# Optimization experiments

Hardware: AMD Instinct MI355X
Metric: run time of the kernel (lower is better)

Reference implementation:

```python
import jax, jax.numpy as jnp
import numpy as np

KEEP_RATIO = 0.5
TEMPERATURE = 1.0
MIN_GATE = 0.0
EPS = 1e-06


def setup_inputs() -> dict:
    key = jax.random.key(0)
    k1, k2 = jax.random.split(key)
    B, C = 8192, 4096
    token = jax.random.normal(k1, (B, C), dtype=jnp.float32)
    proxy = jax.random.normal(k2, (B, C), dtype=jnp.float32)
    return {"token": token, "proxy": proxy}


def reference(token, proxy):
    tok = token  # [B, C]
    px = jax.lax.stop_gradient(proxy)  # detach_proxy=True
    score = jnp.abs(tok * px)  # [B, C]
    B, C = score.shape
    k = max(1, int(round(C * KEEP_RATIO)))
    # hard mask: top-k indices per row -> scatter 1.0
    _, topk_idx = jax.lax.top_k(score, k)  # [B, k]
    rows = jnp.arange(B)[:, None]
    hard_mask = jnp.zeros_like(score).at[rows, topk_idx].set(1.0)
    # per-row standardization (torch.std is unbiased -> ddof=1)
    mu = jnp.mean(score, axis=-1, keepdims=True)
    sigma = jnp.maximum(jnp.std(score, axis=-1, ddof=1, keepdims=True), EPS)
    z = (score - mu) / sigma / max(TEMPERATURE, EPS)
    soft_gate = jax.nn.sigmoid(z)
    if MIN_GATE > 0:
        soft_gate = soft_gate * (1.0 - MIN_GATE) + MIN_GATE
    gate = soft_gate * (1.0 - hard_mask) + hard_mask
    return tok * gate
```

## Files before the change

kernel.cpp:

```cpp
#include <hip/hip_runtime.h>
#include <math.h>

#define CLS   4096
#define KSEL  2048u
#define TPB   256

typedef float f32x4 __attribute__((ext_vector_type(4)));


__device__ __forceinline__ int h0slot(unsigned b) {
    unsigned j = b & 7u, t = b >> 3;
    return (int)((j << 8) | ((t + 4u*j) & 255u));
}

template<int SHIFT, int NBITS, int BPL>
__device__ __forceinline__ void radix_small(const float sc[16], unsigned* hist,
        int lane, unsigned& prefix, unsigned& kr, unsigned& cnt_eq)
{
    const unsigned msk = (1u << NBITS) - 1u;
    #pragma unroll
    for (int i = 0; i < 16; ++i) {
        unsigned u = __float_as_uint(sc[i]);
        if ((u >> (SHIFT + NBITS)) == (prefix >> (SHIFT + NBITS)))
            atomicAdd(&hist[(u >> SHIFT) & msk], 1u);
    }
    __syncthreads();
    unsigned c[BPL];
    if constexpr (BPL == 4) {
        uint4 x = *(const uint4*)&hist[lane * 4];
        c[0] = x.x; c[1] = x.y; c[2] = x.z; c[3] = x.w;
    } else {
        c[0] = hist[lane];
    }
    unsigned sfx[BPL + 1]; sfx[BPL] = 0;
    #pragma unroll
    for (int j = BPL - 1; j >= 0; --j) sfx[j] = sfx[j + 1] + c[j];
    const unsigned tot = sfx[0];
    unsigned s = tot;
    #pragma unroll
    for (int off = 1; off < 64; off <<= 1) {
        unsigned t = __shfl_down(s, off);
        if (lane + off < 64) s += t;
    }
    const unsigned Sx = s - tot;
    const bool has = (Sx < kr) && (kr <= Sx + tot);
    unsigned bin = 0, below = 0, ceq = 0;
    if (has) {
        #pragma unroll
        for (int j = 0; j < BPL; ++j)
            if (Sx + sfx[j] >= kr && Sx + sfx[j + 1] < kr) {
                bin = (unsigned)(lane * BPL + j);
                below = Sx + sfx[j + 1];
                ceq = c[j];
            }
    }
    unsigned long long m = __ballot(has);
    int src = (int)__builtin_ctzll(m);
    bin = __shfl(bin, src); below = __shfl(below, src); ceq = __shfl(ceq, src);
    prefix |= bin << SHIFT;
    kr -= below;
    cnt_eq = ceq;
}

__global__ __launch_bounds__(TPB) void proxy_gate_kernel(
    const float* __restrict__ token,
    const float* __restrict__ proxy,
    float* __restrict__ out)
{
    __shared__ __align__(16) unsigned char lds[18816];
    unsigned* h0    = (unsigned*)(lds);
    unsigned* cand  = (unsigned*)(lds + 16416);
    unsigned* h1    = (unsigned*)(lds + 16416);
    unsigned* h2    = (unsigned*)(lds + 17456);
    unsigned* h3    = (unsigned*)(lds + 18496);
    unsigned* s_cnt = (unsigned*)(lds + 18752);
    unsigned* s_wt  = (unsigned*)(lds + 18756);
    unsigned* s_bc  = (unsigned*)(lds + 18772);
    float*    s_fr  = (float*)   (lds + 18784);
    unsigned char* s_flag = lds;
    unsigned*      s_suf  = (unsigned*)(lds + 8192);

    const int tid  = threadIdx.x;
    const int lane = tid & 63;
    const int wv   = tid >> 6;
    const size_t base = (size_t)blockIdx.x * CLS;
    const float4* t4 = (const float4*)(token + base);
    const float4* p4 = (const float4*)(proxy + base);
    f32x4* o4 = (f32x4*)(out + base);

    float4 tv[4], pv[4];
    #pragma unroll
    for (int i = 0; i < 4; ++i) { tv[i] = t4[i*TPB + tid]; pv[i] = p4[i*TPB + tid]; }
    {
        uint4 z = make_uint4(0u, 0u, 0u, 0u);
        uint4* zp = (uint4*)lds;
        #pragma unroll
        for (int m = 0; m < 5; ++m) { int idx = m*TPB + tid; if (idx < 1154) zp[idx] = z; }
        if (tid == 0) *s_cnt = 0u;
    }

    float tok[16], sc[16];
    float sum = 0.f, sumsq = 0.f;
    #pragma unroll
    for (int i = 0; i < 4; ++i) {
        float a;
        a = fabsf(tv[i].x*pv[i].x); tok[i*4+0]=tv[i].x; sc[i*4+0]=a; sum+=a; sumsq+=a*a;
        a = fabsf(tv[i].y*pv[i].y); tok[i*4+1]=tv[i].y; sc[i*4+1]=a; sum+=a; sumsq+=a*a;
        a = fabsf(tv[i].z*pv[i].z); tok[i*4+2]=tv[i].z; sc[i*4+2]=a; sum+=a; sumsq+=a*a;
        a = fabsf(tv[i].w*pv[i].w); tok[i*4+3]=tv[i].w; sc[i*4+3]=a; sum+=a; sumsq+=a*a;
    }
    __syncthreads();

    {
        unsigned* h0c = h0 + (((tid >> 2) & 1) ? 2052 : 0);
        #pragma unroll
        for (int i = 0; i < 16; ++i)
            atomicAdd(&h0c[h0slot(__float_as_uint(sc[i]) >> 20)], 1u);
    }
    #pragma unroll
    for (int off = 32; off > 0; off >>= 1) {
        sum   += __shfl_xor(sum, off);
        sumsq += __shfl_xor(sumsq, off);
    }
    if (lane == 0) { s_fr[wv] = sum; s_fr[4+wv] = sumsq; }
    __syncthreads();

    const float tot_s = s_fr[0]+s_fr[1]+s_fr[2]+s_fr[3];
    const float tot_q = s_fr[4]+s_fr[5]+s_fr[6]+s_fr[7];
    const float mu = tot_s * (1.0f/CLS);
    float var = (tot_q - tot_s*mu) * (1.0f/(CLS-1));
    var = fmaxf(var, 0.0f);
    const float inv_sigma = 1.0f / fmaxf(sqrtf(var), 1e-6f);

    unsigned kr = KSEL;
    {
        unsigned c[8];
        #pragma unroll
        for (int j = 0; j < 8; ++j) {
            int sl = (j << 8) | ((tid + 4*j) & 255);
            c[j] = h0[sl] + h0[2052 + sl];
        }
        unsigned sfx[9]; sfx[8] = 0;
        #pragma unroll
        for (int j = 7; j >= 0; --j) sfx[j] = sfx[j+1] + c[j];
        const unsigned tot = sfx[0];
        unsigned s = tot;
        #pragma unroll
        for (int off = 1; off < 64; off <<= 1) {
            unsigned t = __shfl_down(s, off);
            if (lane + off < 64) s += t;
        }
        if (lane == 0) s_wt[wv] = s;
        __syncthreads();
        unsigned addhi = 0;
        #pragma unroll
        for (int w2 = 0; w2 < 4; ++w2) if (w2 > wv) addhi += s_wt[w2];
        const unsigned Sx = (s - tot) + addhi;
        if (Sx < kr && kr <= Sx + tot) {
            #pragma unroll
            for (int j = 0; j < 8; ++j)
                if (Sx + sfx[j] >= kr && Sx + sfx[j+1] < kr) {
                    s_bc[0] = (unsigned)(tid*8 + j);
                    s_bc[1] = Sx + sfx[j+1];
                    s_bc[2] = c[j];
                }
        }
        __syncthreads();
        kr -= s_bc[1];
    }
    const unsigned bin = s_bc[0];
    unsigned cnt_eq = s_bc[2];

    {
        unsigned cmask = 0, lc = 0;
        #pragma unroll
        for (int ii = 0; ii < 16; ++ii) {
            bool cnd = ((__float_as_uint(sc[ii]) >> 20) == bin);
            cmask |= ((unsigned)cnd) << ii;
            lc += (unsigned)cnd;
        }
        unsigned inc = lc;
        #pragma unroll
        for (int off = 1; off < 64; off <<= 1) {
            unsigned t = __shfl_up(inc, off);
            if (lane >= off) inc += t;
        }
        const unsigned wtot = __shfl(inc, 63);
        unsigned wbase = 0;
        if (lane == 0) wbase = atomicAdd(s_cnt, wtot);
        wbase = __shfl(wbase, 0);
        unsigned p = wbase + (inc - lc);
        #pragma unroll
        for (int ii = 0; ii < 16; ++ii) {
            if ((cmask >> ii) & 1u) {
                unsigned u = __float_as_uint(sc[ii]);
                unsigned idx = (unsigned)((ii >> 2)*1024 + tid*4 + (ii & 3));
                if (p < 512u) cand[p] = ((u & 0xFFFFFu) << 12) | (4095u - idx);
                ++p;
            }
        }
    }
    __syncthreads();
    const unsigned cnt = *s_cnt;
    const bool cand_mode = (cnt <= 512u);

    float thr = 0.f; bool tie_rare = false;
    if (cand_mode) {
        #pragma unroll
        for (int rpt = 0; rpt < 2; ++rpt) {
            const unsigned slot = (unsigned)tid + (unsigned)rpt*256u;
            if (slot < cnt) {
                const unsigned my = cand[slot];
                unsigned rank = 0;
                const uint4* c4 = (const uint4*)cand;
                const unsigned nq = (cnt + 3u) >> 2;
                for (unsigned q = 0; q < nq; ++q) {
                    uint4 v = c4[q];
                    rank += (unsigned)(v.x > my) + (unsigned)(v.y > my)
                          + (unsigned)(v.z > my) + (unsigned)(v.w > my);
                }
                if (rank == kr - 1u) s_bc[0] = my;
            }
        }
    } else {
        unsigned prefix = bin << 20;
        {
            unsigned* hz = (unsigned*)(lds + 16416);
            #pragma unroll
            for (int m = 0; m < 3; ++m) { int ix = m*TPB + tid; if (ix < 584) hz[ix] = 0u; }
        }
        __syncthreads();
        radix_small<12, 8, 4>(sc, h1, lane, prefix, kr, cnt_eq);
        radix_small< 4, 8, 4>(sc, h2, lane, prefix, kr, cnt_eq);
        radix_small< 0, 4, 1>(sc, h3, lane, prefix, kr, cnt_eq);
        thr = __uint_as_float(prefix);
        tie_rare = (cnt_eq != kr);
        if (tie_rare) {
            #pragma unroll
            for (int i = 0; i < 4; ++i)
                #pragma unroll
                for (int c2 = 0; c2 < 4; ++c2)
                    s_flag[i*1024 + tid*4 + c2] = (sc[i*4+c2] == thr) ? 1 : 0;
            __syncthreads();
            unsigned lc = 0;
            unsigned char mf[16];
            #pragma unroll
            for (int m = 0; m < 16; ++m) { mf[m] = s_flag[tid*16 + m]; lc += mf[m]; }
            s_suf[tid] = lc;
            __syncthreads();
            #pragma unroll
            for (int off = 1; off < 256; off <<= 1) {
                unsigned w = s_suf[tid] + ((tid >= off) ? s_suf[tid - off] : 0u);
                __syncthreads();
                s_suf[tid] = w;
                __syncthreads();
            }
            unsigned r = s_suf[tid] - lc;
            #pragma unroll
            for (int m = 0; m < 16; ++m) {
                if (mf[m]) { s_flag[tid*16 + m] = (r < kr) ? 2 : 0; ++r; }
            }
        }
    }
    __syncthreads();
    const unsigned Kth = s_bc[0];

    #pragma unroll
    for (int i = 0; i < 4; ++i) {
        float res[4];
        #pragma unroll
        for (int c2 = 0; c2 < 4; ++c2) {
            const float s = sc[i*4+c2];
            const float z = (s - mu) * inv_sigma;
            const float soft = 1.0f / (1.0f + __expf(-z));
            bool hard;
            const unsigned u = __float_as_uint(s);
            if (cand_mode) {
                const unsigned e = u >> 20;
                const unsigned idx = (unsigned)(i*1024 + tid*4 + c2);
                const unsigned packed = ((u & 0xFFFFFu) << 12) | (4095u - idx);
                hard = (e > bin) || ((e == bin) && (packed >= Kth));
            } else if (tie_rare) {
                hard = (s > thr) || ((s == thr) && (s_flag[i*1024 + tid*4 + c2] == 2));
            } else {
                hard = (s >= thr);
            }
            res[c2] = tok[i*4+c2] * (hard ? 1.0f : soft);
        }
        f32x4 rv = { res[0], res[1], res[2], res[3] };
        __builtin_nontemporal_store(rv, &o4[i*TPB + tid]);
    }
}

extern "C" void kernel_launch(void* const* d_in, const int* in_sizes, int n_in,
                              void* d_out, int out_size, void* d_ws, size_t ws_size,
                              hipStream_t stream) {
    const float* token = (const float*)d_in[0];
    const float* proxy = (const float*)d_in[1];
    float* outp = (float*)d_out;
    const int B = in_sizes[0] / CLS;
    hipLaunchKernelGGL(proxy_gate_kernel, dim3(B), dim3(TPB), 0, stream,
                       token, proxy, outp);
}
```

Measured before the change: 72.65 us.

## Process eight rows per block with register prefetch of next row

Each block now loops over eight rows instead of one. While the current row is being processed, it loads the next row's token and proxy into registers, so global-memory latency overlaps with the LDS-heavy top-k selection. The grid shrinks from 8192 blocks to 1024, which reduces parallelism and latency hiding across blocks. The extra prefetch registers may also lower occupancy.

Result: slower. 121.1 us (+66.7%).

```diff
diff --git a/kernel.cpp b/kernel.cpp
--- a/kernel.cpp
+++ b/kernel.cpp
@@ -4,6 +4,7 @@
 #define CLS   4096
 #define KSEL  2048u
 #define TPB   256
+#define ROWS  8
 
 typedef float f32x4 __attribute__((ext_vector_type(4)));
 
@@ -65,7 +66,8 @@
 __global__ __launch_bounds__(TPB) void proxy_gate_kernel(
     const float* __restrict__ token,
     const float* __restrict__ proxy,
-    float* __restrict__ out)
+    float* __restrict__ out,
+    int nrows)
 {
     __shared__ __align__(16) unsigned char lds[18816];
     unsigned* h0    = (unsigned*)(lds);
@@ -83,14 +85,15 @@
     const int tid  = threadIdx.x;
     const int lane = tid & 63;
     const int wv   = tid >> 6;
-    const size_t base = (size_t)blockIdx.x * CLS;
-    const float4* t4 = (const float4*)(token + base);
-    const float4* p4 = (const float4*)(proxy + base);
-    f32x4* o4 = (f32x4*)(out + base);
+    const int row0 = blockIdx.x * ROWS;
 
     float4 tv[4], pv[4];
-    #pragma unroll
-    for (int i = 0; i < 4; ++i) { tv[i] = t4[i*TPB + tid]; pv[i] = p4[i*TPB + tid]; }
+    {
+        const float4* t4 = (const float4*)(token + (size_t)row0 * CLS);
+        const float4* p4 = (const float4*)(proxy + (size_t)row0 * CLS);
+        #pragma unroll
+        for (int i = 0; i < 4; ++i) { tv[i] = t4[i*TPB + tid]; pv[i] = p4[i*TPB + tid]; }
+    }
     {
         uint4 z = make_uint4(0u, 0u, 0u, 0u);
         uint4* zp = (uint4*)lds;
@@ -99,196 +102,223 @@
         if (tid == 0) *s_cnt = 0u;
     }
 
-    float tok[16], sc[16];
-    float sum = 0.f, sumsq = 0.f;
-    #pragma unroll
-    for (int i = 0; i < 4; ++i) {
-        float a;
-        a = fabsf(tv[i].x*pv[i].x); tok[i*4+0]=tv[i].x; sc[i*4+0]=a; sum+=a; sumsq+=a*a;
-        a = fabsf(tv[i].y*pv[i].y); tok[i*4+1]=tv[i].y; sc[i*4+1]=a; sum+=a; sumsq+=a*a;
-        a = fabsf(tv[i].z*pv[i].z); tok[i*4+2]=tv[i].z; sc[i*4+2]=a; sum+=a; sumsq+=a*a;
-        a = fabsf(tv[i].w*pv[i].w); tok[i*4+3]=tv[i].w; sc[i*4+3]=a; sum+=a; sumsq+=a*a;
-    }
-    __syncthreads();
-
-    {
-        unsigned* h0c = h0 + (((tid >> 2) & 1) ? 2052 : 0);
-        #pragma unroll
-        for (int i = 0; i < 16; ++i)
-            atomicAdd(&h0c[h0slot(__float_as_uint(sc[i]) >> 20)], 1u);
-    }
-    #pragma unroll
-    for (int off = 32; off > 0; off >>= 1) {
-        sum   += __shfl_xor(sum, off);
-        sumsq += __shfl_xor(sumsq, off);
-    }
-    if (lane == 0) { s_fr[wv] = sum; s_fr[4+wv] = sumsq; }
-    __syncthreads();
-
-    const float tot_s = s_fr[0]+s_fr[1]+s_fr[2]+s_fr[3];
-    const float tot_q = s_fr[4]+s_fr[5]+s_fr[6]+s_fr[7];
-    const float mu = tot_s * (1.0f/CLS);
-    float var = (tot_q - tot_s*mu) * (1.0f/(CLS-1));
-    var = fmaxf(var, 0.0f);
-    const float inv_sigma = 1.0f / fmaxf(sqrtf(var), 1e-6f);
-
-    unsigned kr = KSEL;
-    {
-        unsigned c[8];
-        #pragma unroll
-        for (int j = 0; j < 8; ++j) {
-            int sl = (j << 8) | ((tid + 4*j) & 255);
-            c[j] = h0[sl] + h0[2052 + sl];
-        }
-        unsigned sfx[9]; sfx[8] = 0;
-        #pragma unroll
-        for (int j = 7; j >= 0; --j) sfx[j] = sfx[j+1] + c[j];
-        const unsigned tot = sfx[0];
-        unsigned s = tot;
-        #pragma unroll
-        for (int off = 1; off < 64; off <<= 1) {
-            unsigned t = __shfl_down(s, off);
-            if (lane + off < 64) s += t;
-        }
-        if (lane == 0) s_wt[wv] = s;
+    for (int r = 0; r < ROWS; ++r) {
+        const int row = row0 + r;
+        if (row >= nrows) break;
+        const bool pf = (r + 1 < ROWS) && (row + 1 < nrows);
+
+        float4 ntv[4], npv[4];
+        if (pf) {
+            const float4* t4 = (const float4*)(token + (size_t)(row+1) * CLS);
+            const float4* p4 = (const float4*)(proxy + (size_t)(row+1) * CLS);
+            #pragma unroll
+            for (int i = 0; i < 4; ++i) { ntv[i] = t4[i*TPB + tid]; npv[i] = p4[i*TPB + tid]; }
+        }
+
+        float sc[16];
+        float sum = 0.f, sumsq = 0.f;
+        #pragma unroll
+        for (int i = 0; i < 4; ++i) {
+            float a;
+            a = fabsf(tv[i].x*pv[i].x); sc[i*4+0]=a; sum+=a; sumsq+=a*a;
+            a = fabsf(tv[i].y*pv[i].y); sc[i*4+1]=a; sum+=a; sumsq+=a*a;
+            a = fabsf(tv[i].z*pv[i].z); sc[i*4+2]=a; sum+=a; sumsq+=a*a;
+            a = fabsf(tv[i].w*pv[i].w); sc[i*4+3]=a; sum+=a; sumsq+=a*a;
+        }
         __syncthreads();
-        unsigned addhi = 0;
-        #pragma unroll
-        for (int w2 = 0; w2 < 4; ++w2) if (w2 > wv) addhi += s_wt[w2];
-        const unsigned Sx = (s - tot) + addhi;
-        if (Sx < kr && kr <= Sx + tot) {
-            #pragma unroll
-            for (int j = 0; j < 8; ++j)
-                if (Sx + sfx[j] >= kr && Sx + sfx[j+1] < kr) {
-                    s_bc[0] = (unsigned)(tid*8 + j);
-                    s_bc[1] = Sx + sfx[j+1];
-                    s_bc[2] = c[j];
-                }
-        }
+
+        {
+            unsigned* h0c = h0 + (((tid >> 2) & 1) ? 2052 : 0);
+            #pragma unroll
+            for (int i = 0; i < 16; ++i)
+                atomicAdd(&h0c[h0slot(__float_as_uint(sc[i]) >> 20)], 1u);
+        }
+        #pragma unroll
+        for (int off = 32; off > 0; off >>= 1) {
+            sum   += __shfl_xor(sum, off);
+            sumsq += __shfl_xor(sumsq, off);
+        }
+        if (lane == 0) { s_fr[wv] = sum; s_fr[4+wv] = sumsq; }
         __syncthreads();
-        kr -= s_bc[1];
-    }
-    const unsigned bin = s_bc[0];
-    unsigned cnt_eq = s_bc[2];
-
-    {
-        unsigned cmask = 0, lc = 0;
-        #pragma unroll
-        for (int ii = 0; ii < 16; ++ii) {
-            bool cnd = ((__float_as_uint(sc[ii]) >> 20) == bin);
-            cmask |= ((unsigned)cnd) << ii;
-            lc += (unsigned)cnd;
-        }
-        unsigned inc = lc;
-        #pragma unroll
-        for (int off = 1; off < 64; off <<= 1) {
-            unsigned t = __shfl_up(inc, off);
-            if (lane >= off) inc += t;
-        }
-        const unsigned wtot = __shfl(inc, 63);
-        unsigned wbase = 0;
-        if (lane == 0) wbase = atomicAdd(s_cnt, wtot);
-        wbase = __shfl(wbase, 0);
-        unsigned p = wbase + (inc - lc);
-        #pragma unroll
-        for (int ii = 0; ii < 16; ++ii) {
-            if ((cmask >> ii) & 1u) {
-                unsigned u = __float_as_uint(sc[ii]);
-                unsigned idx = (unsigned)((ii >> 2)*1024 + tid*4 + (ii & 3));
-                if (p < 512u) cand[p] = ((u & 0xFFFFFu) << 12) | (4095u - idx);
-                ++p;
-            }
-        }
-    }
-    __syncthreads();
-    const unsigned cnt = *s_cnt;
-    const bool cand_mode = (cnt <= 512u);
-
-    float thr = 0.f; bool tie_rare = false;
-    if (cand_mode) {
-        #pragma unroll
-        for (int rpt = 0; rpt < 2; ++rpt) {
-            const unsigned slot = (unsigned)tid + (unsigned)rpt*256u;
-            if (slot < cnt) {
-                const unsigned my = cand[slot];
-                unsigned rank = 0;
-                const uint4* c4 = (const uint4*)cand;
-                const unsigned nq = (cnt + 3u) >> 2;
-                for (unsigned q = 0; q < nq; ++q) {
-                    uint4 v = c4[q];
-                    rank += (unsigned)(v.x > my) + (unsigned)(v.y > my)
-                          + (unsigned)(v.z > my) + (unsigned)(v.w > my);
-                }
-                if (rank == kr - 1u) s_bc[0] = my;
-            }
-        }
-    } else {
-        unsigned prefix = bin << 20;
+
+        const float tot_s = s_fr[0]+s_fr[1]+s_fr[2]+s_fr[3];
+        const float tot_q = s_fr[4]+s_fr[5]+s_fr[6]+s_fr[7];
+        const float mu = tot_s * (1.0f/CLS);
+        float var = (tot_q - tot_s*mu) * (1.0f/(CLS-1));
+        var = fmaxf(var, 0.0f);
+        const float inv_sigma = 1.0f / fmaxf(sqrtf(var), 1e-6f);
+
+        unsigned kr = KSEL;
         {
-            unsigned* hz = (unsigned*)(lds + 16416);
-            #pragma unroll
-            for (int m = 0; m < 3; ++m) { int ix = m*TPB + tid; if (ix < 584) hz[ix] = 0u; }
+            unsigned c[8];
+            #pragma unroll
+            for (int j = 0; j < 8; ++j) {
+                int sl = (j << 8) | ((tid + 4*j) & 255);
+                c[j] = h0[sl] + h0[2052 + sl];
+            }
+            unsigned sfx[9]; sfx[8] = 0;
+            #pragma unroll
+            for (int j = 7; j >= 0; --j) sfx[j] = sfx[j+1] + c[j];
+            const unsigned tot = sfx[0];
+            unsigned s = tot;
+            #pragma unroll
+            for (int off = 1; off < 64; off <<= 1) {
+                unsigned t = __shfl_down(s, off);
+                if (lane + off < 64) s += t;
+            }
+            if (lane == 0) s_wt[wv] = s;
+            __syncthreads();
+            unsigned addhi = 0;
+            #pragma unroll
+            for (int w2 = 0; w2 < 4; ++w2) if (w2 > wv) addhi += s_wt[w2];
+            const unsigned Sx = (s - tot) + addhi;
+            if (Sx < kr && kr <= Sx + tot) {
+                #pragma unroll
+                for (int j = 0; j < 8; ++j)
+                    if (Sx + sfx[j] >= kr && Sx + sfx[j+1] < kr) {
+                        s_bc[0] = (unsigned)(tid*8 + j);
+                        s_bc[1] = Sx + sfx[j+1];
+                        s_bc[2] = c[j];
+                    }
+            }
+            __syncthreads();
+            kr -= s_bc[1];
+        }
+        const unsigned bin = s_bc[0];
+        unsigned cnt_eq = s_bc[2];
+
+        {
+            unsigned cmask = 0, lc = 0;
+            #pragma unroll
+            for (int ii = 0; ii < 16; ++ii) {
+                bool cnd = ((__float_as_uint(sc[ii]) >> 20) == bin);
+                cmask |= ((unsigned)cnd) << ii;
+                lc += (unsigned)cnd;
+            }
+            unsigned inc = lc;
+            #pragma unroll
+            for (int off = 1; off < 64; off <<= 1) {
+                unsigned t = __shfl_up(inc, off);
+                if (lane >= off) inc += t;
+            }
+            const unsigned wtot = __shfl(inc, 63);
+            unsigned wbase = 0;
+            if (lane == 0) wbase = atomicAdd(s_cnt, wtot);
+            wbase = __shfl(wbase, 0);
+            unsigned p = wbase + (inc - lc);
+            #pragma unroll
+            for (int ii = 0; ii < 16; ++ii) {
+                if ((cmask >> ii) & 1u) {
+                    unsigned u = __float_as_uint(sc[ii]);
+                    unsigned idx = (unsigned)((ii >> 2)*1024 + tid*4 + (ii & 3));
+                    if (p < 512u) cand[p] = ((u & 0xFFFFFu) << 12) | (4095u - idx);
+                    ++p;
+                }
+            }
         }
         __syncthreads();
-        radix_small<12, 8, 4>(sc, h1, lane, prefix, kr, cnt_eq);
-        radix_small< 4, 8, 4>(sc, h2, lane, prefix, kr, cnt_eq);
-        radix_small< 0, 4, 1>(sc, h3, lane, prefix, kr, cnt_eq);
-        thr = __uint_as_float(prefix);
-        tie_rare = (cnt_eq != kr);
-        if (tie_rare) {
-            #pragma unroll
-            for (int i = 0; i < 4; ++i)
-                #pragma unroll
-                for (int c2 = 0; c2 < 4; ++c2)
-                    s_flag[i*1024 + tid*4 + c2] = (sc[i*4+c2] == thr) ? 1 : 0;
+        const unsigned cnt = *s_cnt;
+        const bool cand_mode = (cnt <= 512u);
+
+        float thr = 0.f; bool tie_rare = false;
+        if (cand_mode) {
+            #pragma unroll
+            for (int rpt = 0; rpt < 2; ++rpt) {
+                const unsigned slot = (unsigned)tid + (unsigned)rpt*256u;
+                if (slot < cnt) {
+                    const unsigned my = cand[slot];
+                    unsigned rank = 0;
+                    const uint4* c4 = (const uint4*)cand;
+                    const unsigned nq = (cnt + 3u) >> 2;
+                    for (unsigned q = 0; q < nq; ++q) {
+                        uint4 v = c4[q];
+                        rank += (unsigned)(v.x > my) + (unsigned)(v.y > my)
+                              + (unsigned)(v.z > my) + (unsigned)(v.w > my);
+                    }
+                    if (rank == kr - 1u) s_bc[0] = my;
+                }
+            }
+        } else {
+            unsigned prefix = bin << 20;
+            {
+                unsigned* hz = (unsigned*)(lds + 16416);
+                #pragma unroll
+                for (int m = 0; m < 3; ++m) { int ix = m*TPB + tid; if (ix < 584) hz[ix] = 0u; }
+            }
             __syncthreads();
-            unsigned lc = 0;
-            unsigned char mf[16];
-            #pragma unroll
-            for (int m = 0; m < 16; ++m) { mf[m] = s_flag[tid*16 + m]; lc += mf[m]; }
-            s_suf[tid] = lc;
-            __syncthreads();
-            #pragma unroll
-            for (int off = 1; off < 256; off <<= 1) {
-                unsigned w = s_suf[tid] + ((tid >= off) ? s_suf[tid - off] : 0u);
+            radix_small<12, 8, 4>(sc, h1, lane, prefix, kr, cnt_eq);
+            radix_small< 4, 8, 4>(sc, h2, lane, prefix, kr, cnt_eq);
+            radix_small< 0, 4, 1>(sc, h3, lane, prefix, kr, cnt_eq);
+            thr = __uint_as_float(prefix);
+            tie_rare = (cnt_eq != kr);
+            if (tie_rare) {
+                #pragma unroll
+                for (int i = 0; i < 4; ++i)
+                    #pragma unroll
+                    for (int c2 = 0; c2 < 4; ++c2)
+                        s_flag[i*1024 + tid*4 + c2] = (sc[i*4+c2] == thr) ? 1 : 0;
                 __syncthreads();
-                s_suf[tid] = w;
+                unsigned lc = 0;
+                unsigned char mf[16];
+                #pragma unroll
+                for (int m = 0; m < 16; ++m) { mf[m] = s_flag[tid*16 + m]; lc += mf[m]; }
+                s_suf[tid] = lc;
                 __syncthreads();
-            }
-            unsigned r = s_suf[tid] - lc;
-            #pragma unroll
-            for (int m = 0; m < 16; ++m) {
-                if (mf[m]) { s_flag[tid*16 + m] = (r < kr) ? 2 : 0; ++r; }
-            }
-        }
-    }
-    __syncthreads();
-    const unsigned Kth = s_bc[0];
-
-    #pragma unroll
-    for (int i = 0; i < 4; ++i) {
-        float res[4];
-        #pragma unroll
-        for (int c2 = 0; c2 < 4; ++c2) {
-            const float s = sc[i*4+c2];
-            const float z = (s - mu) * inv_sigma;
-            const float soft = 1.0f / (1.0f + __expf(-z));
-            bool hard;
-            const unsigned u = __float_as_uint(s);
-            if (cand_mode) {
-                const unsigned e = u >> 20;
-                const unsigned idx = (unsigned)(i*1024 + tid*4 + c2);
-                const unsigned packed = ((u & 0xFFFFFu) << 12) | (4095u - idx);
-                hard = (e > bin) || ((e == bin) && (packed >= Kth));
-            } else if (tie_rare) {
-                hard = (s > thr) || ((s == thr) && (s_flag[i*1024 + tid*4 + c2] == 2));
-            } else {
-                hard = (s >= thr);
-            }
-            res[c2] = tok[i*4+c2] * (hard ? 1.0f : soft);
-        }
-        f32x4 rv = { res[0], res[1], res[2], res[3] };
-        __builtin_nontemporal_store(rv, &o4[i*TPB + tid]);
+                #pragma unroll
+                for (int off = 1; off < 256; off <<= 1) {
+                    unsigned w = s_suf[tid] + ((tid >= off) ? s_suf[tid - off] : 0u);
+                    __syncthreads();
+                    s_suf[tid] = w;
+                    __syncthreads();
+                }
+                unsigned r2 = s_suf[tid] - lc;
+                #pragma unroll
+                for (int m = 0; m < 16; ++m) {
+                    if (mf[m]) { s_flag[tid*16 + m] = (r2 < kr) ? 2 : 0; ++r2; }
+                }
+            }
+        }
+        __syncthreads();
+        const unsigned Kth = s_bc[0];
+
+        f32x4* o4 = (f32x4*)(out + (size_t)row * CLS);
+        #pragma unroll
+        for (int i = 0; i < 4; ++i) {
+            const float tkc[4] = { tv[i].x, tv[i].y, tv[i].z, tv[i].w };
+            f32x4 rv;
+            #pragma unroll
+            for (int c2 = 0; c2 < 4; ++c2) {
+                const float s = sc[i*4+c2];
+                const float z = (s - mu) * inv_sigma;
+                const float soft = 1.0f / (1.0f + __expf(-z));
+                bool hard;
+                const unsigned u = __float_as_uint(s);
+                if (cand_mode) {
+                    const unsigned e = u >> 20;
+                    const unsigned idx = (unsigned)(i*1024 + tid*4 + c2);
+                    const unsigned packed = ((u & 0xFFFFFu) << 12) | (4095u - idx);
+                    hard = (e > bin) || ((e == bin) && (packed >= Kth));
+                } else if (tie_rare) {
+                    hard = (s > thr) || ((s == thr) && (s_flag[i*1024 + tid*4 + c2] == 2));
+                } else {
+                    hard = (s >= thr);
+                }
+                rv[c2] = tkc[c2] * (hard ? 1.0f : soft);
+            }
+            __builtin_nontemporal_store(rv, &o4[i*TPB + tid]);
+        }
+
+        if (!cand_mode) __syncthreads();
+
+        if (pf) {
+            uint4 z = make_uint4(0u, 0u, 0u, 0u);
+            uint4* zp = (uint4*)lds;
+            #pragma unroll
+            for (int m = 0; m < 5; ++m) { int idx = m*TPB + tid; if (idx < 1154) zp[idx] = z; }
+            if (tid == 0) *s_cnt = 0u;
+            #pragma unroll
+            for (int i = 0; i < 4; ++i) { tv[i] = ntv[i]; pv[i] = npv[i]; }
+        }
     }
 }
 
@@ -299,6 +329,7 @@
     const float* proxy = (const float*)d_in[1];
     float* outp = (float*)d_out;
     const int B = in_sizes[0] / CLS;
-    hipLaunchKernelGGL(proxy_gate_kernel, dim3(B), dim3(TPB), 0, stream,
-                       token, proxy, outp);
+    const int nblk = (B + ROWS - 1) / ROWS;
+    hipLaunchKernelGGL(proxy_gate_kernel, dim3(nblk), dim3(TPB), 0, stream,
+                       token, proxy, outp, B);
 }
```

## Use single linear histogram, shrink LDS, and simplify sigmoid and hard-mask compare

Applied to the files above, without the earlier changes.

Replaces the duplicated, swizzled 2-copy 4096-bin histogram with a single linear 2048-bin histogram read as uint4 per thread. This cuts LDS from about 18.8KB to about 10.3KB, which may raise occupancy, and removes the merge of the two copies. It also rewrites the sigmoid as exp2 plus rcp with a folded affine term and uses a 64-bit key compare for candidate-mode membership. The trade-off is more LDS atomic contention on one histogram and slightly lower sigmoid precision.

Result: faster. 66.44 us, median of 2 (-8.5%).

```diff
diff --git a/kernel.cpp b/kernel.cpp
--- a/kernel.cpp
+++ b/kernel.cpp
@@ -7,11 +7,6 @@
 
 typedef float f32x4 __attribute__((ext_vector_type(4)));
 
-
-__device__ __forceinline__ int h0slot(unsigned b) {
-    unsigned j = b & 7u, t = b >> 3;
-    return (int)((j << 8) | ((t + 4u*j) & 255u));
-}
 
 template<int SHIFT, int NBITS, int BPL>
 __device__ __forceinline__ void radix_small(const float sc[16], unsigned* hist,
@@ -67,18 +62,18 @@
     const float* __restrict__ proxy,
     float* __restrict__ out)
 {
-    __shared__ __align__(16) unsigned char lds[18816];
+    __shared__ __align__(16) unsigned char lds[10304];
     unsigned* h0    = (unsigned*)(lds);
-    unsigned* cand  = (unsigned*)(lds + 16416);
-    unsigned* h1    = (unsigned*)(lds + 16416);
-    unsigned* h2    = (unsigned*)(lds + 17456);
-    unsigned* h3    = (unsigned*)(lds + 18496);
-    unsigned* s_cnt = (unsigned*)(lds + 18752);
-    unsigned* s_wt  = (unsigned*)(lds + 18756);
-    unsigned* s_bc  = (unsigned*)(lds + 18772);
-    float*    s_fr  = (float*)   (lds + 18784);
+    unsigned* cand  = (unsigned*)(lds + 8192);
+    unsigned* s_cnt = (unsigned*)(lds + 10240);
+    unsigned* s_wt  = (unsigned*)(lds + 10244);
+    unsigned* s_bc  = (unsigned*)(lds + 10260);
+    float*    s_fr  = (float*)   (lds + 10272);
     unsigned char* s_flag = lds;
-    unsigned*      s_suf  = (unsigned*)(lds + 8192);
+    unsigned*      s_suf  = (unsigned*)(lds + 4096);
+    unsigned*      h1     = (unsigned*)(lds + 5120);
+    unsigned*      h2     = (unsigned*)(lds + 6160);
+    unsigned*      h3     = (unsigned*)(lds + 7200);
 
     const int tid  = threadIdx.x;
     const int lane = tid & 63;
@@ -95,28 +90,25 @@
         uint4 z = make_uint4(0u, 0u, 0u, 0u);
         uint4* zp = (uint4*)lds;
         #pragma unroll
-        for (int m = 0; m < 5; ++m) { int idx = m*TPB + tid; if (idx < 1154) zp[idx] = z; }
+        for (int m = 0; m < 3; ++m) { int idx = m*TPB + tid; if (idx < 640) zp[idx] = z; }
         if (tid == 0) *s_cnt = 0u;
     }
 
-    float tok[16], sc[16];
+    float sc[16];
     float sum = 0.f, sumsq = 0.f;
     #pragma unroll
     for (int i = 0; i < 4; ++i) {
         float a;
-        a = fabsf(tv[i].x*pv[i].x); tok[i*4+0]=tv[i].x; sc[i*4+0]=a; sum+=a; sumsq+=a*a;
-        a = fabsf(tv[i].y*pv[i].y); tok[i*4+1]=tv[i].y; sc[i*4+1]=a; sum+=a; sumsq+=a*a;
-        a = fabsf(tv[i].z*pv[i].z); tok[i*4+2]=tv[i].z; sc[i*4+2]=a; sum+=a; sumsq+=a*a;
-        a = fabsf(tv[i].w*pv[i].w); tok[i*4+3]=tv[i].w; sc[i*4+3]=a; sum+=a; sumsq+=a*a;
-    }
-    __syncthreads();
-
-    {
-        unsigned* h0c = h0 + (((tid >> 2) & 1) ? 2052 : 0);
-        #pragma unroll
-        for (int i = 0; i < 16; ++i)
-            atomicAdd(&h0c[h0slot(__float_as_uint(sc[i]) >> 20)], 1u);
-    }
+        a = fabsf(tv[i].x*pv[i].x); sc[i*4+0]=a; sum+=a; sumsq+=a*a;
+        a = fabsf(tv[i].y*pv[i].y); sc[i*4+1]=a; sum+=a; sumsq+=a*a;
+        a = fabsf(tv[i].z*pv[i].z); sc[i*4+2]=a; sum+=a; sumsq+=a*a;
+        a = fabsf(tv[i].w*pv[i].w); sc[i*4+3]=a; sum+=a; sumsq+=a*a;
+    }
+    __syncthreads();
+
+    #pragma unroll
+    for (int i = 0; i < 16; ++i)
+        atomicAdd(&h0[__float_as_uint(sc[i]) >> 20], 1u);
     #pragma unroll
     for (int off = 32; off > 0; off >>= 1) {
         sum   += __shfl_xor(sum, off);
@@ -134,12 +126,9 @@
 
     unsigned kr = KSEL;
     {
-        unsigned c[8];
-        #pragma unroll
-        for (int j = 0; j < 8; ++j) {
-            int sl = (j << 8) | ((tid + 4*j) & 255);
-            c[j] = h0[sl] + h0[2052 + sl];
-        }
+        uint4 x0 = *(const uint4*)&h0[tid*8];
+        uint4 x1 = *(const uint4*)&h0[tid*8 + 4];
+        unsigned c[8] = { x0.x, x0.y, x0.z, x0.w, x1.x, x1.y, x1.z, x1.w };
         unsigned sfx[9]; sfx[8] = 0;
         #pragma unroll
         for (int j = 7; j >= 0; --j) sfx[j] = sfx[j+1] + c[j];
@@ -195,7 +184,7 @@
             if ((cmask >> ii) & 1u) {
                 unsigned u = __float_as_uint(sc[ii]);
                 unsigned idx = (unsigned)((ii >> 2)*1024 + tid*4 + (ii & 3));
-                if (p < 512u) cand[p] = ((u & 0xFFFFFu) << 12) | (4095u - idx);
+                if (p < 512u) cand[p] = (u << 12) | (4095u - idx);
                 ++p;
             }
         }
@@ -225,7 +214,7 @@
     } else {
         unsigned prefix = bin << 20;
         {
-            unsigned* hz = (unsigned*)(lds + 16416);
+            unsigned* hz = (unsigned*)(lds + 5120);
             #pragma unroll
             for (int m = 0; m < 3; ++m) { int ix = m*TPB + tid; if (ix < 584) hz[ix] = 0u; }
         }
@@ -255,39 +244,43 @@
                 s_suf[tid] = w;
                 __syncthreads();
             }
-            unsigned r = s_suf[tid] - lc;
+            unsigned r2 = s_suf[tid] - lc;
             #pragma unroll
             for (int m = 0; m < 16; ++m) {
-                if (mf[m]) { s_flag[tid*16 + m] = (r < kr) ? 2 : 0; ++r; }
-            }
-        }
-    }
-    __syncthreads();
-    const unsigned Kth = s_bc[0];
-
+                if (mf[m]) { s_flag[tid*16 + m] = (r2 < kr) ? 2 : 0; ++r2; }
+            }
+        }
+    }
+    __syncthreads();
+    const unsigned long long Kth64 =
+        ((unsigned long long)bin << 32) | (unsigned long long)s_bc[0];
+
+    const float A  = -inv_sigma * 1.44269504f;
+    const float Bc = -mu * A;
+    const unsigned rbase = 1023u - 4u*(unsigned)tid;
     #pragma unroll
     for (int i = 0; i < 4; ++i) {
-        float res[4];
+        const float tkc[4] = { tv[i].x, tv[i].y, tv[i].z, tv[i].w };
+        f32x4 rv;
         #pragma unroll
         for (int c2 = 0; c2 < 4; ++c2) {
             const float s = sc[i*4+c2];
-            const float z = (s - mu) * inv_sigma;
-            const float soft = 1.0f / (1.0f + __expf(-z));
+            const float e2 = __builtin_amdgcn_exp2f(fmaf(s, A, Bc));
+            const float soft = __builtin_amdgcn_rcpf(1.0f + e2);
+            const unsigned u = __float_as_uint(s);
             bool hard;
-            const unsigned u = __float_as_uint(s);
             if (cand_mode) {
-                const unsigned e = u >> 20;
-                const unsigned idx = (unsigned)(i*1024 + tid*4 + c2);
-                const unsigned packed = ((u & 0xFFFFFu) << 12) | (4095u - idx);
-                hard = (e > bin) || ((e == bin) && (packed >= Kth));
+                const unsigned long long key =
+                    ((unsigned long long)(u >> 20) << 32)
+                    | (unsigned long long)((u << 12) | (rbase + (3u-(unsigned)i)*1024u - (unsigned)c2));
+                hard = (key >= Kth64);
             } else if (tie_rare) {
                 hard = (s > thr) || ((s == thr) && (s_flag[i*1024 + tid*4 + c2] == 2));
             } else {
                 hard = (s >= thr);
             }
-            res[c2] = tok[i*4+c2] * (hard ? 1.0f : soft);
-        }
-        f32x4 rv = { res[0], res[1], res[2], res[3] };
+            rv[c2] = tkc[c2] * (hard ? 1.0f : soft);
+        }
         __builtin_nontemporal_store(rv, &o4[i*TPB + tid]);
     }
 }
```
